# Optimization experiments

Hardware: AMD Instinct MI355X
Metric: run time of the kernel (lower is better)

## Reference

```python
import jax, jax.numpy as jnp
import numpy as np

N_NODES = 50000
N_EDGES = 600000
IN_DIM = 512
HIDDEN = 128
OUT_DIM = 64
N_LAYERS = 3
EPS = 0.1


def setup_inputs() -> dict:
    key = jax.random.key(0)
    ks = jax.random.split(key, 8)
    x = jax.random.normal(ks[0], (N_NODES, IN_DIM), jnp.float32)
    edge_index = jax.random.randint(ks[1], (2, N_EDGES), 0, N_NODES, jnp.int32)
    # xavier-normal-ish scaled weights
    t1_w = jax.random.normal(ks[2], (HIDDEN, IN_DIM), jnp.float32) * (1.414 * (2.0 / (IN_DIM + HIDDEN)) ** 0.5)
    t1_b = jnp.zeros((HIDDEN,), jnp.float32)
    t2_w = jax.random.normal(ks[3], (OUT_DIM, HIDDEN), jnp.float32) * (1.414 * (2.0 / (HIDDEN + OUT_DIM)) ** 0.5)
    t2_b = jnp.zeros((OUT_DIM,), jnp.float32)
    # per-layer FAConv attention vectors: Linear(hidden, 1, bias=False)
    att_l = jax.random.normal(ks[4], (N_LAYERS, HIDDEN), jnp.float32) * 0.1
    att_r = jax.random.normal(ks[5], (N_LAYERS, HIDDEN), jnp.float32) * 0.1
    return dict(x=x, edge_index=edge_index, t1_w=t1_w, t1_b=t1_b,
                t2_w=t2_w, t2_b=t2_b, att_l=att_l, att_r=att_r)


def _gcn_norm(src, dst, n):
    # symmetric gcn_norm without self-loops (as FAConv uses): deg over targets
    deg = jax.ops.segment_sum(jnp.ones(src.shape, jnp.float32), dst, num_segments=n)
    dinv = jnp.where(deg > 0, 1.0 / jnp.sqrt(jnp.maximum(deg, 1.0)), 0.0)
    return dinv[src] * dinv[dst]  # [E]


def _fa_conv(h, raw, src, dst, al_w, ar_w, norm, n):
    # alpha = tanh(att_l . x_j + att_r . x_i), message = x_j * alpha * norm
    al = h @ al_w  # [N]
    ar = h @ ar_w  # [N]
    alpha = jnp.tanh(al[src] + ar[dst])  # [E]
    msg = h[src] * (alpha * norm)[:, None]  # [E, HIDDEN]
    out = jax.ops.segment_sum(msg, dst, num_segments=n)
    return out + EPS * raw


def reference(x, edge_index, t1_w, t1_b, t2_w, t2_b, att_l, att_r):
    src, dst = edge_index[0], edge_index[1]
    n = x.shape[0]
    norm = _gcn_norm(src, dst, n)
    h = jax.nn.relu(x @ t1_w.T + t1_b)  # dropout is identity in eval mode
    raw = h
    for i in range(N_LAYERS):
        h = _fa_conv(h, raw, src, dst, att_l[i], att_r[i], norm, n)
    emb = h @ t2_w.T + t2_b
    out = jax.nn.log_softmax(emb, axis=1)
    return out, emb
```

## Files before the change

### kernel.cpp

```cpp
#include <hip/hip_runtime.h>
#include <hip/hip_bf16.h>
#include <stdint.h>

#define NN 50000
#define NE 600000
#define IN_DIM 512
#define HID 128
#define ODIM 64
#define EPSV 0.1f
#define NBLK ((NN + 255) / 256)

typedef __attribute__((ext_vector_type(8))) short short8;
typedef __attribute__((ext_vector_type(4))) float f32x4;

__device__ __forceinline__ ushort f2bf(float f) {
    union { float f; uint32_t i; } v; v.f = f;
    uint32_t lsb = (v.i >> 16) & 1u;
    uint32_t r = v.i + 0x7fffu + lsb;
    return (ushort)(r >> 16);
}

__device__ __forceinline__ float bf2f(ushort u) {
    union { uint32_t i; float f; } v; v.i = ((uint32_t)u) << 16;
    return v.f;
}

__device__ __forceinline__ short8 pack8(float4 lo, float4 hi) {
    short8 r;
    r[0] = (short)f2bf(lo.x); r[1] = (short)f2bf(lo.y);
    r[2] = (short)f2bf(lo.z); r[3] = (short)f2bf(lo.w);
    r[4] = (short)f2bf(hi.x); r[5] = (short)f2bf(hi.y);
    r[6] = (short)f2bf(hi.z); r[7] = (short)f2bf(hi.w);
    return r;
}

__device__ __forceinline__ float fast_tanh(float z) {
    z = fminf(fmaxf(z, -15.f), 15.f);
    float t = __expf(2.f * z);
    return __fdividef(t - 1.f, t + 1.f);
}

__global__ __launch_bounds__(256) void deg_kernel(const int* __restrict__ dst, int* __restrict__ deg) {
    int e = blockIdx.x * 256 + threadIdx.x;
    if (e < NE) atomicAdd(&deg[dst[e]], 1);
}

__global__ __launch_bounds__(256) void scanA_kernel(const int* __restrict__ deg,
                                                    int* __restrict__ localScan,
                                                    int* __restrict__ blockSums,
                                                    float* __restrict__ dinv) {
    __shared__ int tmp[256];
    int t = threadIdx.x;
    int i = blockIdx.x * 256 + t;
    int v = (i < NN) ? deg[i] : 0;
    tmp[t] = v;
    __syncthreads();
    for (int off = 1; off < 256; off <<= 1) {
        int add = (t >= off) ? tmp[t - off] : 0;
        __syncthreads();
        tmp[t] += add;
        __syncthreads();
    }
    if (i < NN) {
        localScan[i] = tmp[t] - v;
        dinv[i] = (v > 0) ? (1.0f / sqrtf((float)v)) : 0.0f;
    }
    if (t == 255) blockSums[blockIdx.x] = tmp[255];
}

__global__ __launch_bounds__(256) void scanB_kernel(const int* __restrict__ blockSums,
                                                    int* __restrict__ blockOff) {
    __shared__ int tmp[256];
    int t = threadIdx.x;
    int v = (t < NBLK) ? blockSums[t] : 0;
    tmp[t] = v;
    __syncthreads();
    for (int off = 1; off < 256; off <<= 1) {
        int add = (t >= off) ? tmp[t - off] : 0;
        __syncthreads();
        tmp[t] += add;
        __syncthreads();
    }
    blockOff[t] = tmp[t] - v;
}

__global__ __launch_bounds__(256) void scanC_kernel(const int* __restrict__ localScan,
                                                    const int* __restrict__ blockOff,
                                                    int* __restrict__ rowptr,
                                                    int* __restrict__ cursor) {
    int i = blockIdx.x * 256 + threadIdx.x;
    if (i < NN) {
        int v = localScan[i] + blockOff[blockIdx.x];
        rowptr[i] = v;
        cursor[i] = v;
    }
    if (i == 0) rowptr[NN] = NE;
}

__global__ __launch_bounds__(256) void fill_kernel(const int* __restrict__ src, const int* __restrict__ dst,
                                                   int* __restrict__ cursor, int* __restrict__ csr_src) {
    int e = blockIdx.x * 256 + threadIdx.x;
    if (e < NE) {
        int d = dst[e];
        int slot = atomicAdd(&cursor[d], 1);
        csr_src[slot] = src[e];
    }
}

__global__ __launch_bounds__(256) void cvtw_kernel(const float* __restrict__ w, ushort* __restrict__ wbf) {
    int i = blockIdx.x * 256 + threadIdx.x;
    if (i < HID * IN_DIM) wbf[i] = f2bf(w[i]);
}

__global__ __launch_bounds__(1024, 4) void gemm1_kernel(const float* __restrict__ x,
                                                        const ushort* __restrict__ wbf,
                                                        const float* __restrict__ b,
                                                        const float* __restrict__ attl,
                                                        const float* __restrict__ attr,
                                                        const float* __restrict__ dinv,
                                                        float* __restrict__ h,
                                                        float2* __restrict__ AD,
                                                        float* __restrict__ AR) {
    __shared__ __attribute__((aligned(16))) ushort b_sm[HID * IN_DIM];
    int t = threadIdx.x;
    int wv = __builtin_amdgcn_readfirstlane(t >> 6);
    int lane = t & 63;
    int m0 = blockIdx.x * 256;

    {
        uint4 bg[8];
#pragma unroll
        for (int rnd = 0; rnd < 8; ++rnd)
            bg[rnd] = *(const uint4*)(wbf + (size_t)(rnd * 1024 + t) * 8);
#pragma unroll
        for (int rnd = 0; rnd < 8; ++rnd) {
            int G = rnd * 1024 + t;
            int row = G >> 6;
            int g = G & 63;
            *(uint4*)&b_sm[(size_t)((row << 6) | (g ^ (row & 7))) * 8] = bg[rnd];
        }
    }
    __syncthreads();

    int rsel = lane & 15;
    int koff = (lane >> 4) * 8;
    int sw = rsel & 7;
    int qg = koff >> 3;
    int row = m0 + wv * 16 + rsel; if (row >= NN) row = NN - 1;
    const float* xr = x + (size_t)row * IN_DIM + koff;

    f32x4 acc[8];
#pragma unroll
    for (int tt = 0; tt < 8; ++tt) acc[tt] = (f32x4){0.f, 0.f, 0.f, 0.f};

    float4 c0lo = *(const float4*)(xr);
    float4 c0hi = *(const float4*)(xr + 4);
    float4 c1lo = *(const float4*)(xr + 32);
    float4 c1hi = *(const float4*)(xr + 36);

#pragma unroll
    for (int ks = 0; ks < 16; ks += 2) {
        float4 n0lo, n0hi, n1lo, n1hi;
        bool more = (ks + 2 < 16);
        if (more) {
            n0lo = *(const float4*)(xr + (ks + 2) * 32);
            n0hi = *(const float4*)(xr + (ks + 2) * 32 + 4);
            n1lo = *(const float4*)(xr + (ks + 3) * 32);
            n1hi = *(const float4*)(xr + (ks + 3) * 32 + 4);
        }
        short8 a0 = pack8(c0lo, c0hi);
#pragma unroll
        for (int tt = 0; tt < 8; ++tt) {
            int rb = tt * 16 + rsel;
            short8 bf = *(const short8*)&b_sm[(size_t)(rb << 9) + (size_t)(((ks * 4 + qg) ^ sw) << 3)];
            acc[tt] = __builtin_amdgcn_mfma_f32_16x16x32_bf16(a0, bf, acc[tt], 0, 0, 0);
        }
        short8 a1 = pack8(c1lo, c1hi);
#pragma unroll
        for (int tt = 0; tt < 8; ++tt) {
            int rb = tt * 16 + rsel;
            short8 bf = *(const short8*)&b_sm[(size_t)(rb << 9) + (size_t)((((ks + 1) * 4 + qg) ^ sw) << 3)];
            acc[tt] = __builtin_amdgcn_mfma_f32_16x16x32_bf16(a1, bf, acc[tt], 0, 0, 0);
        }
        if (more) { c0lo = n0lo; c0hi = n0hi; c1lo = n1lo; c1hi = n1hi; }
    }

    int rbase = (lane >> 4) * 4;
    int col0 = lane & 15;
    float alv[8], arv[8], bias[8];
#pragma unroll
    for (int tt = 0; tt < 8; ++tt) {
        alv[tt]  = attl[tt * 16 + col0];
        arv[tt]  = attr[tt * 16 + col0];
        bias[tt] = b[tt * 16 + col0];
    }
#pragma unroll
    for (int r = 0; r < 4; ++r) {
        int rrow = m0 + wv * 16 + rbase + r;
        float p = 0.f, q = 0.f;
#pragma unroll
        for (int tt = 0; tt < 8; ++tt) {
            float v = acc[tt][r] + bias[tt];
            v = v > 0.f ? v : 0.f;
            if (rrow < NN) h[(size_t)rrow * HID + tt * 16 + col0] = v;
            p += v * alv[tt];
            q += v * arv[tt];
        }
#pragma unroll
        for (int off = 8; off; off >>= 1) { p += __shfl_xor(p, off); q += __shfl_xor(q, off); }
        if (col0 == 0 && rrow < NN) {
            float2 vv; vv.x = p; vv.y = dinv[rrow];
            AD[rrow] = vv;
            AR[rrow] = q;
        }
    }
}

__global__ __launch_bounds__(256) void agg_kernel(const float* __restrict__ h,
                                                  const float* __restrict__ raw,
                                                  float* __restrict__ hn,
                                                  const int* __restrict__ rowptr,
                                                  const int* __restrict__ csr_src,
                                                  const float* __restrict__ dinv,
                                                  const float2* __restrict__ AD,
                                                  const float* __restrict__ AR,
                                                  const float* __restrict__ attl_next,
                                                  const float* __restrict__ attr_next,
                                                  float2* __restrict__ ADout,
                                                  float* __restrict__ ARout) {
    int wv = __builtin_amdgcn_readfirstlane(threadIdx.x >> 6);
    int lane = threadIdx.x & 63;
    int d = blockIdx.x * 4 + wv;
    if (d >= NN) return;
    const float2* h2 = (const float2*)h;
    float ar_d = AR[d];
    float dinv_d = dinv[d];
    float2 rawd = ((const float2*)raw)[(size_t)d * 64 + lane];
    float accx = EPSV * rawd.x, accy = EPSV * rawd.y;
    int e = rowptr[d], e1 = rowptr[d + 1];
    for (; e + 8 <= e1; e += 8) {
        int sv = csr_src[e + (lane & 7)];
        int s0 = __builtin_amdgcn_readfirstlane(__shfl(sv, 0));
        int s1 = __builtin_amdgcn_readfirstlane(__shfl(sv, 1));
        int s2 = __builtin_amdgcn_readfirstlane(__shfl(sv, 2));
        int s3 = __builtin_amdgcn_readfirstlane(__shfl(sv, 3));
        int s4 = __builtin_amdgcn_readfirstlane(__shfl(sv, 4));
        int s5 = __builtin_amdgcn_readfirstlane(__shfl(sv, 5));
        int s6 = __builtin_amdgcn_readfirstlane(__shfl(sv, 6));
        int s7 = __builtin_amdgcn_readfirstlane(__shfl(sv, 7));
        float2 ad0 = AD[s0], ad1 = AD[s1], ad2 = AD[s2], ad3 = AD[s3];
        float2 ad4 = AD[s4], ad5 = AD[s5], ad6 = AD[s6], ad7 = AD[s7];
        float2 v0 = h2[(size_t)s0 * 64 + lane];
        float2 v1 = h2[(size_t)s1 * 64 + lane];
        float2 v2 = h2[(size_t)s2 * 64 + lane];
        float2 v3 = h2[(size_t)s3 * 64 + lane];
        float2 v4 = h2[(size_t)s4 * 64 + lane];
        float2 v5 = h2[(size_t)s5 * 64 + lane];
        float2 v6 = h2[(size_t)s6 * 64 + lane];
        float2 v7 = h2[(size_t)s7 * 64 + lane];
        float w0 = fast_tanh(ad0.x + ar_d) * ad0.y * dinv_d;
        float w1 = fast_tanh(ad1.x + ar_d) * ad1.y * dinv_d;
        float w2 = fast_tanh(ad2.x + ar_d) * ad2.y * dinv_d;
        float w3 = fast_tanh(ad3.x + ar_d) * ad3.y * dinv_d;
        float w4 = fast_tanh(ad4.x + ar_d) * ad4.y * dinv_d;
        float w5 = fast_tanh(ad5.x + ar_d) * ad5.y * dinv_d;
        float w6 = fast_tanh(ad6.x + ar_d) * ad6.y * dinv_d;
        float w7 = fast_tanh(ad7.x + ar_d) * ad7.y * dinv_d;
        accx += w0 * v0.x + w1 * v1.x + w2 * v2.x + w3 * v3.x;
        accy += w0 * v0.y + w1 * v1.y + w2 * v2.y + w3 * v3.y;
        accx += w4 * v4.x + w5 * v5.x + w6 * v6.x + w7 * v7.x;
        accy += w4 * v4.y + w5 * v5.y + w6 * v6.y + w7 * v7.y;
    }
    for (; e + 4 <= e1; e += 4) {
        int sv = csr_src[e + (lane & 3)];
        int s0 = __builtin_amdgcn_readfirstlane(__shfl(sv, 0));
        int s1 = __builtin_amdgcn_readfirstlane(__shfl(sv, 1));
        int s2 = __builtin_amdgcn_readfirstlane(__shfl(sv, 2));
        int s3 = __builtin_amdgcn_readfirstlane(__shfl(sv, 3));
        float2 ad0 = AD[s0], ad1 = AD[s1], ad2 = AD[s2], ad3 = AD[s3];
        float2 v0 = h2[(size_t)s0 * 64 + lane];
        float2 v1 = h2[(size_t)s1 * 64 + lane];
        float2 v2 = h2[(size_t)s2 * 64 + lane];
        float2 v3 = h2[(size_t)s3 * 64 + lane];
        float w0 = fast_tanh(ad0.x + ar_d) * ad0.y * dinv_d;
        float w1 = fast_tanh(ad1.x + ar_d) * ad1.y * dinv_d;
        float w2 = fast_tanh(ad2.x + ar_d) * ad2.y * dinv_d;
        float w3 = fast_tanh(ad3.x + ar_d) * ad3.y * dinv_d;
        accx += w0 * v0.x + w1 * v1.x + w2 * v2.x + w3 * v3.x;
        accy += w0 * v0.y + w1 * v1.y + w2 * v2.y + w3 * v3.y;
    }
    for (; e < e1; ++e) {
        int s = __builtin_amdgcn_readfirstlane(csr_src[e]);
        float2 ad = AD[s];
        float2 v = h2[(size_t)s * 64 + lane];
        float w = fast_tanh(ad.x + ar_d) * ad.y * dinv_d;
        accx += w * v.x;
        accy += w * v.y;
    }
    float2 o; o.x = accx; o.y = accy;
    ((float2*)hn)[(size_t)d * 64 + lane] = o;
    if (attl_next) {
        float al0 = attl_next[2 * lane], al1 = attl_next[2 * lane + 1];
        float ar0 = attr_next[2 * lane], ar1 = attr_next[2 * lane + 1];
        float p = accx * al0 + accy * al1;
        float q = accx * ar0 + accy * ar1;
#pragma unroll
        for (int off = 32; off; off >>= 1) { p += __shfl_xor(p, off); q += __shfl_xor(q, off); }
        if (lane == 0) {
            float2 v; v.x = p; v.y = dinv_d;
            ADout[d] = v;
            ARout[d] = q;
        }
    }
}

__global__ __launch_bounds__(256) void head_kernel(const float* __restrict__ h,
                                                   const float* __restrict__ w2,
                                                   const float* __restrict__ b2,
                                                   float* __restrict__ out) {
    __shared__ __attribute__((aligned(16))) ushort bhi_sm[ODIM * HID];
    __shared__ __attribute__((aligned(16))) ushort blo_sm[ODIM * HID];
    int t = threadIdx.x;
    int wv = __builtin_amdgcn_readfirstlane(t >> 6);
    int lane = t & 63;

    {
        int j = t >> 2;
        int k0 = (t & 3) * 32;
        const float* wr = w2 + (size_t)j * HID + k0;
#pragma unroll
        for (int gg = 0; gg < 4; ++gg) {
            float4 a4 = *(const float4*)(wr + gg * 8);
            float4 b4 = *(const float4*)(wr + gg * 8 + 4);
            float vals[8] = {a4.x, a4.y, a4.z, a4.w, b4.x, b4.y, b4.z, b4.w};
            short8 vhi, vlo;
#pragma unroll
            for (int e = 0; e < 8; ++e) {
                ushort hu = f2bf(vals[e]);
                ushort lu = f2bf(vals[e] - bf2f(hu));
                vhi[e] = (short)hu; vlo[e] = (short)lu;
            }
            int g = (t & 3) * 4 + gg;
            int p = g ^ (j & 7);
            *(short8*)&bhi_sm[(size_t)j * HID + p * 8] = vhi;
            *(short8*)&blo_sm[(size_t)j * HID + p * 8] = vlo;
        }
    }
    __syncthreads();

    int rsel = lane & 15;
    int q16 = lane >> 4;
    int koff = q16 * 8;
    int sw = rsel & 7;
    int m0 = blockIdx.x * 128 + wv * 32;

    f32x4 acc[2][4];
#pragma unroll
    for (int ms = 0; ms < 2; ++ms)
#pragma unroll
        for (int nt = 0; nt < 4; ++nt) acc[ms][nt] = (f32x4){0.f, 0.f, 0.f, 0.f};

#pragma unroll
    for (int ks = 0; ks < 4; ++ks) {
        short8 ahi[2], alo[2];
#pragma unroll
        for (int ms = 0; ms < 2; ++ms) {
            int row = m0 + ms * 16 + rsel; if (row >= NN) row = NN - 1;
            const float* hr = h + (size_t)row * HID + ks * 32 + koff;
            float4 p0 = *(const float4*)hr;
            float4 p1 = *(const float4*)(hr + 4);
            float vals[8] = {p0.x, p0.y, p0.z, p0.w, p1.x, p1.y, p1.z, p1.w};
#pragma unroll
            for (int e = 0; e < 8; ++e) {
                ushort hu = f2bf(vals[e]);
                ushort lu = f2bf(vals[e] - bf2f(hu));
                ahi[ms][e] = (short)hu; alo[ms][e] = (short)lu;
            }
        }
        int p = (ks * 4 + q16) ^ sw;
#pragma unroll
        for (int nt = 0; nt < 4; ++nt) {
            size_t bofs = (size_t)(nt * 16 + rsel) * HID + p * 8;
            short8 bh = *(const short8*)&bhi_sm[bofs];
            short8 bl = *(const short8*)&blo_sm[bofs];
#pragma unroll
            for (int ms = 0; ms < 2; ++ms) {
                acc[ms][nt] = __builtin_amdgcn_mfma_f32_16x16x32_bf16(ahi[ms], bh, acc[ms][nt], 0, 0, 0);
                acc[ms][nt] = __builtin_amdgcn_mfma_f32_16x16x32_bf16(alo[ms], bh, acc[ms][nt], 0, 0, 0);
                acc[ms][nt] = __builtin_amdgcn_mfma_f32_16x16x32_bf16(ahi[ms], bl, acc[ms][nt], 0, 0, 0);
            }
        }
    }

    int col0 = lane & 15;
    float bias[4];
#pragma unroll
    for (int nt = 0; nt < 4; ++nt) bias[nt] = b2[nt * 16 + col0];
#pragma unroll
    for (int ms = 0; ms < 2; ++ms) {
#pragma unroll
        for (int r = 0; r < 4; ++r) {
            int node = m0 + ms * 16 + q16 * 4 + r;
            float v0 = acc[ms][0][r] + bias[0];
            float v1 = acc[ms][1][r] + bias[1];
            float v2 = acc[ms][2][r] + bias[2];
            float v3 = acc[ms][3][r] + bias[3];
            float m = fmaxf(fmaxf(v0, v1), fmaxf(v2, v3));
#pragma unroll
            for (int off = 8; off; off >>= 1) m = fmaxf(m, __shfl_xor(m, off));
            float s = __expf(v0 - m) + __expf(v1 - m) + __expf(v2 - m) + __expf(v3 - m);
#pragma unroll
            for (int off = 8; off; off >>= 1) s += __shfl_xor(s, off);
            float ls = m + __logf(s);
            if (node < NN) {
                out[(size_t)node * ODIM + 0 * 16 + col0] = v0 - ls;
                out[(size_t)node * ODIM + 1 * 16 + col0] = v1 - ls;
                out[(size_t)node * ODIM + 2 * 16 + col0] = v2 - ls;
                out[(size_t)node * ODIM + 3 * 16 + col0] = v3 - ls;
                size_t eb = (size_t)NN * ODIM + (size_t)node * ODIM;
                out[eb + 0 * 16 + col0] = v0;
                out[eb + 1 * 16 + col0] = v1;
                out[eb + 2 * 16 + col0] = v2;
                out[eb + 3 * 16 + col0] = v3;
            }
        }
    }
}

extern "C" void kernel_launch(void* const* d_in, const int* in_sizes, int n_in,
                              void* d_out, int out_size, void* d_ws, size_t ws_size,
                              hipStream_t stream) {
    const float* x    = (const float*)d_in[0];
    const int*   ei   = (const int*)d_in[1];
    const float* t1w  = (const float*)d_in[2];
    const float* t1b  = (const float*)d_in[3];
    const float* t2w  = (const float*)d_in[4];
    const float* t2b  = (const float*)d_in[5];
    const float* attl = (const float*)d_in[6];
    const float* attr = (const float*)d_in[7];
    float* out = (float*)d_out;

    const int* src = ei;
    const int* dst = ei + NE;

    char* ws = (char*)d_ws;
    size_t off = 0;
    auto alloc = [&](size_t bytes) { char* p = ws + off; off += (bytes + 255) & ~(size_t)255; return p; };
    float*  hA   = (float*)alloc((size_t)NN * HID * 4);
    float*  hB   = (float*)alloc((size_t)NN * HID * 4);
    float*  hC   = (float*)alloc((size_t)NN * HID * 4);
    ushort* wbf  = (ushort*)alloc((size_t)HID * IN_DIM * 2);
    int*    deg  = (int*)alloc((size_t)NN * 4);
    float*  dinv = (float*)alloc((size_t)NN * 4);
    int*    rowptr = (int*)alloc((size_t)(NN + 1) * 4);
    int*    cursor = (int*)alloc((size_t)NN * 4);
    int*    csr_src = (int*)alloc((size_t)NE * 4);
    int*    localScan = (int*)alloc((size_t)NN * 4);
    int*    blockSums = (int*)alloc((size_t)256 * 4);
    int*    blockOff  = (int*)alloc((size_t)256 * 4);
    float2* AD_A = (float2*)alloc((size_t)NN * 8);
    float*  AR_A = (float*)alloc((size_t)NN * 4);
    float2* AD_B = (float2*)alloc((size_t)NN * 8);
    float*  AR_B = (float*)alloc((size_t)NN * 4);
    (void)ws_size;

    hipMemsetAsync(deg, 0, (size_t)NN * 4, stream);

    dim3 blk(256);
    deg_kernel<<<(NE + 255) / 256, blk, 0, stream>>>(dst, deg);
    scanA_kernel<<<NBLK, blk, 0, stream>>>(deg, localScan, blockSums, dinv);
    scanB_kernel<<<1, blk, 0, stream>>>(blockSums, blockOff);
    scanC_kernel<<<NBLK, blk, 0, stream>>>(localScan, blockOff, rowptr, cursor);
    fill_kernel<<<(NE + 255) / 256, blk, 0, stream>>>(src, dst, cursor, csr_src);

    cvtw_kernel<<<(HID * IN_DIM + 255) / 256, blk, 0, stream>>>(t1w, wbf);
    gemm1_kernel<<<(NN + 255) / 256, dim3(1024), 0, stream>>>(x, wbf, t1b,
                                                              attl + 0 * HID, attr + 0 * HID,
                                                              dinv, hA, AD_A, AR_A);

    agg_kernel<<<(NN + 3) / 4, blk, 0, stream>>>(hA, hA, hB, rowptr, csr_src, dinv,
                                                 AD_A, AR_A, attl + 1 * HID, attr + 1 * HID, AD_B, AR_B);
    agg_kernel<<<(NN + 3) / 4, blk, 0, stream>>>(hB, hA, hC, rowptr, csr_src, dinv,
                                                 AD_B, AR_B, attl + 2 * HID, attr + 2 * HID, AD_A, AR_A);
    agg_kernel<<<(NN + 3) / 4, blk, 0, stream>>>(hC, hA, hB, rowptr, csr_src, dinv,
                                                 AD_A, AR_A, nullptr, nullptr, nullptr, nullptr);

    head_kernel<<<(NN + 127) / 128, blk, 0, stream>>>(hB, t2w, t2b, out);
}
```

Baseline: 413.9 us.

## Store hidden features in bf16 for gathers and head GEMM

New measurement: 378.0 us. 1.1x faster.

```diff
diff --git a/kernel.cpp b/kernel.cpp
--- a/kernel.cpp
+++ b/kernel.cpp
@@ -23,6 +23,13 @@
 __device__ __forceinline__ float bf2f(ushort u) {
     union { uint32_t i; float f; } v; v.i = ((uint32_t)u) << 16;
     return v.f;
+}
+
+__device__ __forceinline__ float bflo(uint32_t u) {
+    union { uint32_t i; float f; } v; v.i = u << 16; return v.f;
+}
+__device__ __forceinline__ float bfhi(uint32_t u) {
+    union { uint32_t i; float f; } v; v.i = u & 0xffff0000u; return v.f;
 }
 
 __device__ __forceinline__ short8 pack8(float4 lo, float4 hi) {
@@ -119,6 +126,7 @@
                                                         const float* __restrict__ attr,
                                                         const float* __restrict__ dinv,
                                                         float* __restrict__ h,
+                                                        ushort* __restrict__ hb,
                                                         float2* __restrict__ AD,
                                                         float* __restrict__ AR) {
     __shared__ __attribute__((aligned(16))) ushort b_sm[HID * IN_DIM];
@@ -202,7 +210,10 @@
         for (int tt = 0; tt < 8; ++tt) {
             float v = acc[tt][r] + bias[tt];
             v = v > 0.f ? v : 0.f;
-            if (rrow < NN) h[(size_t)rrow * HID + tt * 16 + col0] = v;
+            if (rrow < NN) {
+                h[(size_t)rrow * HID + tt * 16 + col0] = v;
+                hb[(size_t)rrow * HID + tt * 16 + col0] = f2bf(v);
+            }
             p += v * alv[tt];
             q += v * arv[tt];
         }
@@ -216,9 +227,9 @@
     }
 }
 
-__global__ __launch_bounds__(256) void agg_kernel(const float* __restrict__ h,
+__global__ __launch_bounds__(256) void agg_kernel(const ushort* __restrict__ hb,
                                                   const float* __restrict__ raw,
-                                                  float* __restrict__ hn,
+                                                  ushort* __restrict__ hnb,
                                                   const int* __restrict__ rowptr,
                                                   const int* __restrict__ csr_src,
                                                   const float* __restrict__ dinv,
@@ -232,7 +243,7 @@
     int lane = threadIdx.x & 63;
     int d = blockIdx.x * 4 + wv;
     if (d >= NN) return;
-    const float2* h2 = (const float2*)h;
+    const uint32_t* h4 = (const uint32_t*)hb;
     float ar_d = AR[d];
     float dinv_d = dinv[d];
     float2 rawd = ((const float2*)raw)[(size_t)d * 64 + lane];
@@ -250,14 +261,14 @@
         int s7 = __builtin_amdgcn_readfirstlane(__shfl(sv, 7));
         float2 ad0 = AD[s0], ad1 = AD[s1], ad2 = AD[s2], ad3 = AD[s3];
         float2 ad4 = AD[s4], ad5 = AD[s5], ad6 = AD[s6], ad7 = AD[s7];
-        float2 v0 = h2[(size_t)s0 * 64 + lane];
-        float2 v1 = h2[(size_t)s1 * 64 + lane];
-        float2 v2 = h2[(size_t)s2 * 64 + lane];
-        float2 v3 = h2[(size_t)s3 * 64 + lane];
-        float2 v4 = h2[(size_t)s4 * 64 + lane];
-        float2 v5 = h2[(size_t)s5 * 64 + lane];
-        float2 v6 = h2[(size_t)s6 * 64 + lane];
-        float2 v7 = h2[(size_t)s7 * 64 + lane];
+        uint32_t u0 = h4[(size_t)s0 * 64 + lane];
+        uint32_t u1 = h4[(size_t)s1 * 64 + lane];
+        uint32_t u2 = h4[(size_t)s2 * 64 + lane];
+        uint32_t u3 = h4[(size_t)s3 * 64 + lane];
+        uint32_t u4 = h4[(size_t)s4 * 64 + lane];
+        uint32_t u5 = h4[(size_t)s5 * 64 + lane];
+        uint32_t u6 = h4[(size_t)s6 * 64 + lane];
+        uint32_t u7 = h4[(size_t)s7 * 64 + lane];
         float w0 = fast_tanh(ad0.x + ar_d) * ad0.y * dinv_d;
         float w1 = fast_tanh(ad1.x + ar_d) * ad1.y * dinv_d;
         float w2 = fast_tanh(ad2.x + ar_d) * ad2.y * dinv_d;
@@ -266,10 +277,10 @@
         float w5 = fast_tanh(ad5.x + ar_d) * ad5.y * dinv_d;
         float w6 = fast_tanh(ad6.x + ar_d) * ad6.y * dinv_d;
         float w7 = fast_tanh(ad7.x + ar_d) * ad7.y * dinv_d;
-        accx += w0 * v0.x + w1 * v1.x + w2 * v2.x + w3 * v3.x;
-        accy += w0 * v0.y + w1 * v1.y + w2 * v2.y + w3 * v3.y;
-        accx += w4 * v4.x + w5 * v5.x + w6 * v6.x + w7 * v7.x;
-        accy += w4 * v4.y + w5 * v5.y + w6 * v6.y + w7 * v7.y;
+        accx += w0 * bflo(u0) + w1 * bflo(u1) + w2 * bflo(u2) + w3 * bflo(u3);
+        accy += w0 * bfhi(u0) + w1 * bfhi(u1) + w2 * bfhi(u2) + w3 * bfhi(u3);
+        accx += w4 * bflo(u4) + w5 * bflo(u5) + w6 * bflo(u6) + w7 * bflo(u7);
+        accy += w4 * bfhi(u4) + w5 * bfhi(u5) + w6 * bfhi(u6) + w7 * bfhi(u7);
     }
     for (; e + 4 <= e1; e += 4) {
         int sv = csr_src[e + (lane & 3)];
@@ -278,27 +289,27 @@
         int s2 = __builtin_amdgcn_readfirstlane(__shfl(sv, 2));
         int s3 = __builtin_amdgcn_readfirstlane(__shfl(sv, 3));
         float2 ad0 = AD[s0], ad1 = AD[s1], ad2 = AD[s2], ad3 = AD[s3];
-        float2 v0 = h2[(size_t)s0 * 64 + lane];
-        float2 v1 = h2[(size_t)s1 * 64 + lane];
-        float2 v2 = h2[(size_t)s2 * 64 + lane];
-        float2 v3 = h2[(size_t)s3 * 64 + lane];
+        uint32_t u0 = h4[(size_t)s0 * 64 + lane];
+        uint32_t u1 = h4[(size_t)s1 * 64 + lane];
+        uint32_t u2 = h4[(size_t)s2 * 64 + lane];
+        uint32_t u3 = h4[(size_t)s3 * 64 + lane];
         float w0 = fast_tanh(ad0.x + ar_d) * ad0.y * dinv_d;
         float w1 = fast_tanh(ad1.x + ar_d) * ad1.y * dinv_d;
         float w2 = fast_tanh(ad2.x + ar_d) * ad2.y * dinv_d;
         float w3 = fast_tanh(ad3.x + ar_d) * ad3.y * dinv_d;
-        accx += w0 * v0.x + w1 * v1.x + w2 * v2.x + w3 * v3.x;
-        accy += w0 * v0.y + w1 * v1.y + w2 * v2.y + w3 * v3.y;
+        accx += w0 * bflo(u0) + w1 * bflo(u1) + w2 * bflo(u2) + w3 * bflo(u3);
+        accy += w0 * bfhi(u0) + w1 * bfhi(u1) + w2 * bfhi(u2) + w3 * bfhi(u3);
     }
     for (; e < e1; ++e) {
         int s = __builtin_amdgcn_readfirstlane(csr_src[e]);
         float2 ad = AD[s];
-        float2 v = h2[(size_t)s * 64 + lane];
+        uint32_t u = h4[(size_t)s * 64 + lane];
         float w = fast_tanh(ad.x + ar_d) * ad.y * dinv_d;
-        accx += w * v.x;
-        accy += w * v.y;
-    }
-    float2 o; o.x = accx; o.y = accy;
-    ((float2*)hn)[(size_t)d * 64 + lane] = o;
+        accx += w * bflo(u);
+        accy += w * bfhi(u);
+    }
+    ((uint32_t*)hnb)[(size_t)d * 64 + lane] =
+        (uint32_t)f2bf(accx) | ((uint32_t)f2bf(accy) << 16);
     if (attl_next) {
         float al0 = attl_next[2 * lane], al1 = attl_next[2 * lane + 1];
         float ar0 = attr_next[2 * lane], ar1 = attr_next[2 * lane + 1];
@@ -314,7 +325,7 @@
     }
 }
 
-__global__ __launch_bounds__(256) void head_kernel(const float* __restrict__ h,
+__global__ __launch_bounds__(256) void head_kernel(const ushort* __restrict__ hb,
                                                    const float* __restrict__ w2,
                                                    const float* __restrict__ b2,
                                                    float* __restrict__ out) {
@@ -362,20 +373,11 @@
 
 #pragma unroll
     for (int ks = 0; ks < 4; ++ks) {
-        short8 ahi[2], alo[2];
+        short8 a[2];
 #pragma unroll
         for (int ms = 0; ms < 2; ++ms) {
             int row = m0 + ms * 16 + rsel; if (row >= NN) row = NN - 1;
-            const float* hr = h + (size_t)row * HID + ks * 32 + koff;
-            float4 p0 = *(const float4*)hr;
-            float4 p1 = *(const float4*)(hr + 4);
-            float vals[8] = {p0.x, p0.y, p0.z, p0.w, p1.x, p1.y, p1.z, p1.w};
-#pragma unroll
-            for (int e = 0; e < 8; ++e) {
-                ushort hu = f2bf(vals[e]);
-                ushort lu = f2bf(vals[e] - bf2f(hu));
-                ahi[ms][e] = (short)hu; alo[ms][e] = (short)lu;
-            }
+            a[ms] = *(const short8*)(hb + (size_t)row * HID + ks * 32 + koff);
         }
         int p = (ks * 4 + q16) ^ sw;
 #pragma unroll
@@ -385,9 +387,8 @@
             short8 bl = *(const short8*)&blo_sm[bofs];
 #pragma unroll
             for (int ms = 0; ms < 2; ++ms) {
-                acc[ms][nt] = __builtin_amdgcn_mfma_f32_16x16x32_bf16(ahi[ms], bh, acc[ms][nt], 0, 0, 0);
-                acc[ms][nt] = __builtin_amdgcn_mfma_f32_16x16x32_bf16(alo[ms], bh, acc[ms][nt], 0, 0, 0);
-                acc[ms][nt] = __builtin_amdgcn_mfma_f32_16x16x32_bf16(ahi[ms], bl, acc[ms][nt], 0, 0, 0);
+                acc[ms][nt] = __builtin_amdgcn_mfma_f32_16x16x32_bf16(a[ms], bh, acc[ms][nt], 0, 0, 0);
+                acc[ms][nt] = __builtin_amdgcn_mfma_f32_16x16x32_bf16(a[ms], bl, acc[ms][nt], 0, 0, 0);
             }
         }
     }
@@ -447,8 +448,10 @@
     size_t off = 0;
     auto alloc = [&](size_t bytes) { char* p = ws + off; off += (bytes + 255) & ~(size_t)255; return p; };
     float*  hA   = (float*)alloc((size_t)NN * HID * 4);
-    float*  hB   = (float*)alloc((size_t)NN * HID * 4);
-    float*  hC   = (float*)alloc((size_t)NN * HID * 4);
+    ushort* h0b  = (ushort*)alloc((size_t)NN * HID * 2);
+    ushort* h1b  = (ushort*)alloc((size_t)NN * HID * 2);
+    ushort* h2b  = (ushort*)alloc((size_t)NN * HID * 2);
+    ushort* h3b  = (ushort*)alloc((size_t)NN * HID * 2);
     ushort* wbf  = (ushort*)alloc((size_t)HID * IN_DIM * 2);
     int*    deg  = (int*)alloc((size_t)NN * 4);
     float*  dinv = (float*)alloc((size_t)NN * 4);
@@ -476,14 +479,14 @@
     cvtw_kernel<<<(HID * IN_DIM + 255) / 256, blk, 0, stream>>>(t1w, wbf);
     gemm1_kernel<<<(NN + 255) / 256, dim3(1024), 0, stream>>>(x, wbf, t1b,
                                                               attl + 0 * HID, attr + 0 * HID,
-                                                              dinv, hA, AD_A, AR_A);
-
-    agg_kernel<<<(NN + 3) / 4, blk, 0, stream>>>(hA, hA, hB, rowptr, csr_src, dinv,
+                                                              dinv, hA, h0b, AD_A, AR_A);
+
+    agg_kernel<<<(NN + 3) / 4, blk, 0, stream>>>(h0b, hA, h1b, rowptr, csr_src, dinv,
                                                  AD_A, AR_A, attl + 1 * HID, attr + 1 * HID, AD_B, AR_B);
-    agg_kernel<<<(NN + 3) / 4, blk, 0, stream>>>(hB, hA, hC, rowptr, csr_src, dinv,
+    agg_kernel<<<(NN + 3) / 4, blk, 0, stream>>>(h1b, hA, h2b, rowptr, csr_src, dinv,
                                                  AD_B, AR_B, attl + 2 * HID, attr + 2 * HID, AD_A, AR_A);
-    agg_kernel<<<(NN + 3) / 4, blk, 0, stream>>>(hC, hA, hB, rowptr, csr_src, dinv,
+    agg_kernel<<<(NN + 3) / 4, blk, 0, stream>>>(h2b, hA, h3b, rowptr, csr_src, dinv,
                                                  AD_A, AR_A, nullptr, nullptr, nullptr, nullptr);
 
-    head_kernel<<<(NN + 127) / 128, blk, 0, stream>>>(hB, t2w, t2b, out);
-}
+    head_kernel<<<(NN + 127) / 128, blk, 0, stream>>>(h3b, t2w, t2b, out);
+}
```
